# Optimization experiments

Hardware: AMD Instinct MI355X
Metric: run time of the kernel (lower is better)

The kernel has to match this reference:

```python
import jax, jax.numpy as jnp
import numpy as np

N, M, NBR = 20000, 12, 64
AF, ORIG, H, B, K = 256, 92, 256, 200, 50
N_CONV = 3
EPS = 1e-5


def _bn_train(x, gamma, beta):
    mu = x.mean(0)
    var = x.var(0)  # biased, matches torch BN normalization in train mode
    return (x - mu) * jax.lax.rsqrt(var + EPS) * gamma + beta


def _conv_layer(atom_in, nbr_fea, nbr_idx, w1, b1, w2, b2, gamma, beta):
    n, m = nbr_idx.shape
    m1 = m // 2
    atom_nbr = atom_in[nbr_idx]                     # [N, M, AF]
    atom_u = jnp.broadcast_to(atom_in[:, None, :], (n, m1, atom_in.shape[-1]))
    an1, an2 = atom_nbr[:, :m1], atom_nbr[:, m1:]
    nf1, nf2 = nbr_fea[:, :m1], nbr_fea[:, m1:]
    u1 = jnp.concatenate([atom_u, an1, nf1], axis=2)  # [N, M1, 2*AF+NBR]
    u2 = jnp.concatenate([atom_u, an2, nf2], axis=2)
    g1 = jax.nn.relu(jnp.einsum('nmf,fo->nmo', u1, w1) + b1)
    g2 = jax.nn.softplus(jnp.einsum('nmf,fo->nmo', u2, w1) + b1)
    nbr_sumed = g1.sum(1) + g2.sum(1)               # sum over all M neighbors, [N, 2*AF]
    nbr_sumed = nbr_sumed @ w2 + b2                 # [N, AF]
    nbr_sumed = _bn_train(nbr_sumed, gamma, beta)
    return jax.nn.softplus(atom_in + nbr_sumed)


def setup_inputs() -> dict:
    key = jax.random.key(0)
    ks = jax.random.split(key, 16)
    inp = {
        'atom_fea': jax.random.normal(ks[0], (N, ORIG), jnp.float32),
        'nbr_fea': jax.random.normal(ks[1], (N, M, NBR), jnp.float32),
        'nbr_fea_idx': jax.random.randint(ks[2], (N, M), 0, N),
        'M1_index': jax.random.randint(ks[3], (B * K,), 0, N),
        'seg_ids': jnp.repeat(jnp.arange(B), K),
        'm2_fea': jax.random.normal(ks[4], (B, 4), jnp.float32),
        'emb_w': jax.random.normal(ks[5], (ORIG, AF), jnp.float32) * 0.05,
        'emb_b': jnp.zeros((AF,), jnp.float32),
        'w1': jax.random.normal(ks[6], (N_CONV, 2 * AF + NBR, 2 * AF), jnp.float32) * 0.05,
        'b1': jnp.zeros((N_CONV, 2 * AF), jnp.float32),
        'w2': jax.random.normal(ks[7], (N_CONV, 2 * AF, AF), jnp.float32) * 0.05,
        'b2': jnp.zeros((N_CONV, AF), jnp.float32),
        'gamma': jnp.ones((N_CONV, AF), jnp.float32),
        'beta': jnp.zeros((N_CONV, AF), jnp.float32),
        'fc_w': jax.random.normal(ks[8], (AF + 4, H), jnp.float32) * 0.05,
        'fc_b': jnp.zeros((H,), jnp.float32),
        'out_w': jax.random.normal(ks[9], (H, 1), jnp.float32) * 0.05,
        'out_b': jnp.zeros((1,), jnp.float32),
    }
    return inp


def reference(atom_fea, nbr_fea, nbr_fea_idx, M1_index, seg_ids, m2_fea,
              emb_w, emb_b, w1, b1, w2, b2, gamma, beta,
              fc_w, fc_b, out_w, out_b):
    x = jax.nn.softplus(atom_fea @ emb_w + emb_b)           # [N, AF]
    for i in range(N_CONV):
        x = _conv_layer(x, nbr_fea, nbr_fea_idx, w1[i], b1[i], w2[i], b2[i], gamma[i], beta[i])
    m1_fea = x[M1_index]                                    # [B*K, AF]
    sums = jax.ops.segment_sum(m1_fea, seg_ids, num_segments=B)
    counts = jax.ops.segment_sum(jnp.ones((m1_fea.shape[0], 1), m1_fea.dtype), seg_ids, num_segments=B)
    crys = sums / counts                                    # per-crystal mean, [B, AF]
    crys = jnp.concatenate([crys, m2_fea], axis=1)          # [B, AF+4]
    h = jax.nn.softplus(jax.nn.softplus(crys) @ fc_w + fc_b)
    out = h @ out_w + out_b                                 # [B, 1]
    return out
```

## Files before the change

### kernel.cpp

```cpp
#include <hip/hip_runtime.h>
#include <hip/hip_bf16.h>


#define N_ATOM 20000
#define AF     256
#define F2     512
#define ORIG   92
#define ORIG_P 96
#define BB     200
#define KK     50
#define BN_EPS 1e-5f
#define ZS2    268

#define OFF_B1   0
#define OFF_B2   1536
#define OFF_GAM  2304
#define OFF_BET  3072
#define OFF_EMBB 3840
#define OFF_FCB  4096
#define OFF_FCW  4352
#define OFF_OW   70912
#define OFF_OB   71168
#define OFF_M2   71169
#define N_SMALL  71969

#define S_AF   (N_ATOM * ORIG_P)
#define S_EMB  (AF * ORIG_P)
#define S_W12  (3 * 1024 * 256)
#define S_W1F  (3 * 512 * 64)
#define S_W2   (3 * AF * F2)
#define S_SM   N_SMALL
#define S_TOT  (S_AF + S_EMB + S_W12 + S_W1F + S_W2 + S_SM)

using bf16x8 = __attribute__((ext_vector_type(8))) short;
using f32x4  = __attribute__((ext_vector_type(4))) float;

__device__ __forceinline__ float bf2f(__hip_bfloat16 v) { return __bfloat162float(v); }
__device__ __forceinline__ __hip_bfloat16 f2bf(float v) { return __float2bfloat16(v); }
__device__ __forceinline__ unsigned short f2bfbits(float f) {
    unsigned u = __float_as_uint(f);
    u += 0x7fffu + ((u >> 16) & 1u);
    return (unsigned short)(u >> 16);
}
__device__ __forceinline__ float bfbits2f(unsigned short u) {
    return __uint_as_float(((unsigned)u) << 16);
}
__device__ __forceinline__ float softplus_f(float x) {
    return fmaxf(x, 0.f) + __logf(1.f + __expf(-fabsf(x)));
}
__device__ __forceinline__ float ld_any(const void* p, long idx, bool isf32) {
    return isf32 ? ((const float*)p)[idx] : bf2f(((const __hip_bfloat16*)p)[idx]);
}

__global__ void detect_dtype(const unsigned* __restrict__ gamma_raw,
                             unsigned* __restrict__ flag) {
    unsigned u = gamma_raw[0];
    flag[0] = ((u & 0xFFFFu) == 0u) ? 1u : 0u;
}

__global__ __launch_bounds__(256) void prep_nf(const void* __restrict__ nf,
                                               const unsigned* __restrict__ dflag,
                                               unsigned* __restrict__ out) {
    bool isf32 = dflag[0] != 0u;
    int idx = blockIdx.x * 256 + threadIdx.x;
    if (idx >= N_ATOM * 12 * 64 / 4) return;
    if (isf32) {
        float4 v = ((const float4*)nf)[idx];
        out[idx * 2]     = (unsigned)f2bfbits(v.x) | ((unsigned)f2bfbits(v.y) << 16);
        out[idx * 2 + 1] = (unsigned)f2bfbits(v.z) | ((unsigned)f2bfbits(v.w) << 16);
    } else {
        ((uint2*)out)[idx] = ((const uint2*)nf)[idx];
    }
}

__global__ __launch_bounds__(256)
void prep_all(const void* af, const void* emb_w, const void* w1, const void* w2,
              const void* b1, const void* b2, const void* gam, const void* bet,
              const void* embb, const void* fcb, const void* fcw,
              const void* ow, const void* ob, const void* m2,
              const unsigned* __restrict__ dflag,
              __hip_bfloat16* __restrict__ af_pad, __hip_bfloat16* __restrict__ embT,
              __hip_bfloat16* __restrict__ w1T2, __hip_bfloat16* __restrict__ w1Tf,
              __hip_bfloat16* __restrict__ w2T, __hip_bfloat16* __restrict__ smalls) {
    bool isf32 = dflag[0] != 0u;
    int i = blockIdx.x * 256 + threadIdx.x;
    if (i < S_AF) {
        int r = i / ORIG_P, k = i - r * ORIG_P;
        af_pad[i] = (k < ORIG) ? f2bf(ld_any(af, (long)r * ORIG + k, isf32)) : f2bf(0.f);
        return;
    }
    i -= S_AF;
    if (i < S_EMB) {
        int n = i / ORIG_P, k = i - n * ORIG_P;
        embT[i] = (k < ORIG) ? f2bf(ld_any(emb_w, (long)k * AF + n, isf32)) : f2bf(0.f);
        return;
    }
    i -= S_EMB;
    if (i < S_W12) {
        int l = i / (1024 * 256); int rem = i - l * (1024 * 256);
        int c = rem / 256, k = rem - c * 256;
        long src = (c < 512) ? ((long)(l * 576 + k) * F2 + c)
                             : ((long)(l * 576 + 256 + k) * F2 + (c - 512));
        w1T2[i] = f2bf(ld_any(w1, src, isf32));
        return;
    }
    i -= S_W12;
    if (i < S_W1F) {
        int l = i / (512 * 64); int rem = i - l * (512 * 64);
        int c = rem / 64, k = rem - c * 64;
        w1Tf[i] = f2bf(ld_any(w1, (long)(l * 576 + 512 + k) * F2 + c, isf32));
        return;
    }
    i -= S_W1F;
    if (i < S_W2) {
        int l = i / (AF * F2); int rem = i - l * (AF * F2);
        int n = rem / F2, k = rem - n * F2;
        w2T[i] = f2bf(ld_any(w2, (long)(l * F2 + k) * AF + n, isf32));
        return;
    }
    i -= S_W2;
    if (i >= S_SM) return;
    float v;
    if      (i < OFF_B2)   v = ld_any(b1,   i - OFF_B1,  isf32);
    else if (i < OFF_GAM)  v = ld_any(b2,   i - OFF_B2,  isf32);
    else if (i < OFF_BET)  v = ld_any(gam,  i - OFF_GAM, isf32);
    else if (i < OFF_EMBB) v = ld_any(bet,  i - OFF_BET, isf32);
    else if (i < OFF_FCB)  v = ld_any(embb, i - OFF_EMBB,isf32);
    else if (i < OFF_OW)   v = (i < OFF_FCW) ? ld_any(fcb, i - OFF_FCB, isf32)
                                             : ld_any(fcw, i - OFF_FCW, isf32);
    else if (i < OFF_OB)   v = ld_any(ow,   i - OFF_OW,  isf32);
    else if (i < OFF_M2)   v = ld_any(ob,   i - OFF_OB,  isf32);
    else                   v = ld_any(m2,   i - OFF_M2,  isf32);
    smalls[i] = f2bf(v);
}

template <bool OUT_BF16>
__global__ __launch_bounds__(256)
void gemm_kernel(const __hip_bfloat16* __restrict__ A, int lda,
                 const __hip_bfloat16* __restrict__ BT, int ldb,
                 void* __restrict__ Cp, int M, int ldc, int K,
                 const __hip_bfloat16* __restrict__ bias, int act,
                 float* __restrict__ st) {
    __shared__ __align__(16) unsigned short sA[128 * 40];
    __shared__ __align__(16) unsigned short sB[128 * 40];
    __shared__ float sS[128], sS2[128];
    int tid  = threadIdx.x;
    int mt   = blockIdx.x, nt = blockIdx.y;
    int wave = tid >> 6, lane = tid & 63, q = lane >> 4, ln = lane & 15;
    int wr   = wave >> 1, wc = wave & 1;

    if (st && tid < 128) { sS[tid] = 0.f; sS2[tid] = 0.f; }

    f32x4 acc[4][4];
    for (int i = 0; i < 4; i++)
        for (int j = 0; j < 4; j++) acc[i][j] = (f32x4){0.f, 0.f, 0.f, 0.f};

    for (int k0 = 0; k0 < K; k0 += 32) {
        for (int i = tid; i < 512; i += 256) {
            int r = i >> 2, ch = i & 3;
            int row = mt * 128 + r;
            uint4 va = make_uint4(0u, 0u, 0u, 0u);
            if (row < M) va = *(const uint4*)(A + (size_t)row * lda + k0 + ch * 8);
            *(uint4*)(&sA[r * 40 + ch * 8]) = va;
            int n = nt * 128 + r;
            uint4 vb = *(const uint4*)(BT + (size_t)n * ldb + k0 + ch * 8);
            *(uint4*)(&sB[r * 40 + ch * 8]) = vb;
        }
        __syncthreads();
        bf16x8 af[4], bf[4];
        for (int i = 0; i < 4; i++)
            af[i] = *(const bf16x8*)(&sA[(wr * 64 + i * 16 + ln) * 40 + q * 8]);
        for (int j = 0; j < 4; j++)
            bf[j] = *(const bf16x8*)(&sB[(wc * 64 + j * 16 + ln) * 40 + q * 8]);
        for (int i = 0; i < 4; i++)
            for (int j = 0; j < 4; j++)
                acc[i][j] = __builtin_amdgcn_mfma_f32_16x16x32_bf16(af[i], bf[j], acc[i][j], 0, 0, 0);
        __syncthreads();
    }
    for (int j = 0; j < 4; j++) {
        int cl  = wc * 64 + j * 16 + ln;
        int col = nt * 128 + cl;
        float bv = bias ? bf2f(bias[col]) : 0.f;
        float ls = 0.f, ls2 = 0.f;
        for (int i = 0; i < 4; i++) {
            for (int r = 0; r < 4; r++) {
                int row = mt * 128 + wr * 64 + i * 16 + q * 4 + r;
                if (row >= M) continue;
                float v = acc[i][j][r] + bv;
                if (st) { ls += v; ls2 += v * v; }
                if (act == 1) v = softplus_f(v);
                if (OUT_BF16) ((__hip_bfloat16*)Cp)[(size_t)row * ldc + col] = f2bf(v);
                else          ((float*)Cp)[(size_t)row * ldc + col] = v;
            }
        }
        if (st) { atomicAdd(&sS[cl], ls); atomicAdd(&sS2[cl], ls2); }
    }
    if (st) {
        __syncthreads();
        if (tid < 128) {
            int col = nt * 128 + tid;
            atomicAdd(&st[col], sS[tid]);
            atomicAdd(&st[AF + col], sS2[tid]);
        }
    }
}

__global__ __launch_bounds__(256)
void conv_fused(const void* __restrict__ nf,
                const unsigned* __restrict__ dflag,
                int prepped,
                const int* __restrict__ nidx,
                const __hip_bfloat16* __restrict__ xay,
                const __hip_bfloat16* __restrict__ b1l,
                const __hip_bfloat16* __restrict__ w1TfL,
                __hip_bfloat16* __restrict__ ns)
{
    __shared__ __align__(16) unsigned short sNF[48 * 72];
    __shared__ __align__(16) unsigned short sZ[48 * ZS2];
    __shared__ int sIdx[48];

    int tid = threadIdx.x;
    int ab  = blockIdx.x * 4;

    if (prepped || dflag[0] == 0u) {
        const __hip_bfloat16* nfB = (const __hip_bfloat16*)nf;
        for (int i = tid; i < 48 * 8; i += 256) {
            int r = i >> 3, ch = i & 7;
            uint4 v = *(const uint4*)(nfB + (size_t)(ab * 12 + r) * 64 + ch * 8);
            *(uint4*)(&sNF[r * 72 + ch * 8]) = v;
        }
    } else {
        const float* nfF = (const float*)nf;
        for (int i = tid; i < 48 * 8; i += 256) {
            int r = i >> 3, ch = i & 7;
            const float* src = nfF + (size_t)(ab * 12 + r) * 64 + ch * 8;
            float4 v0 = *(const float4*)(src);
            float4 v1 = *(const float4*)(src + 4);
            unsigned short* d = &sNF[r * 72 + ch * 8];
            d[0] = f2bfbits(v0.x); d[1] = f2bfbits(v0.y);
            d[2] = f2bfbits(v0.z); d[3] = f2bfbits(v0.w);
            d[4] = f2bfbits(v1.x); d[5] = f2bfbits(v1.y);
            d[6] = f2bfbits(v1.z); d[7] = f2bfbits(v1.w);
        }
    }
    if (tid < 48) sIdx[tid] = nidx[ab * 12 + tid];
    __syncthreads();

    int wave = tid >> 6, lane = tid & 63, q = lane >> 4, ln = lane & 15;
    int c0 = wave * 32;
    int a = wave, half = lane >> 5, lc = lane & 31;
    int n = ab + a;
    int zc = half * 128 + lc * 4;

    for (int tp = 0; tp < 2; tp++) {
        if (tp) __syncthreads();
        for (int t2 = 0; t2 < 2; t2++) {
            int cb = (tp * 2 + t2) * 128;
            bf16x8 bfr[2][2];
            for (int c2 = 0; c2 < 2; c2++)
                for (int ks = 0; ks < 2; ks++)
                    bfr[c2][ks] = *(const bf16x8*)(w1TfL +
                        (size_t)(cb + c0 + c2 * 16 + ln) * 64 + ks * 32 + q * 8);
            f32x4 acc[3][2];
            for (int rt = 0; rt < 3; rt++)
                for (int c2 = 0; c2 < 2; c2++) acc[rt][c2] = (f32x4){0.f, 0.f, 0.f, 0.f};
            for (int rt = 0; rt < 3; rt++) {
                bf16x8 a0 = *(const bf16x8*)(&sNF[(rt * 16 + ln) * 72 + q * 8]);
                bf16x8 a1 = *(const bf16x8*)(&sNF[(rt * 16 + ln) * 72 + 32 + q * 8]);
                acc[rt][0] = __builtin_amdgcn_mfma_f32_16x16x32_bf16(a0, bfr[0][0], acc[rt][0], 0, 0, 0);
                acc[rt][0] = __builtin_amdgcn_mfma_f32_16x16x32_bf16(a1, bfr[0][1], acc[rt][0], 0, 0, 0);
                acc[rt][1] = __builtin_amdgcn_mfma_f32_16x16x32_bf16(a0, bfr[1][0], acc[rt][1], 0, 0, 0);
                acc[rt][1] = __builtin_amdgcn_mfma_f32_16x16x32_bf16(a1, bfr[1][1], acc[rt][1], 0, 0, 0);
            }
            for (int rt = 0; rt < 3; rt++)
                for (int c2 = 0; c2 < 2; c2++)
                    for (int r = 0; r < 4; r++)
                        sZ[(rt * 16 + q * 4 + r) * ZS2 + t2 * 128 + c0 + c2 * 16 + ln] =
                            f2bfbits(acc[rt][c2][r]);
        }
        __syncthreads();

        int gc = tp * 256 + zc;
        uint2 xau = *(const uint2*)(xay + (size_t)n * 1024 + gc);
        uint2 b1u = *(const uint2*)(b1l + gc);
        float xa0 = bfbits2f((unsigned short)(xau.x & 0xffff)) +
                    bfbits2f((unsigned short)(b1u.x & 0xffff));
        float xa1 = bfbits2f((unsigned short)(xau.x >> 16)) +
                    bfbits2f((unsigned short)(b1u.x >> 16));
        float xa2 = bfbits2f((unsigned short)(xau.y & 0xffff)) +
                    bfbits2f((unsigned short)(b1u.y & 0xffff));
        float xa3 = bfbits2f((unsigned short)(xau.y >> 16)) +
                    bfbits2f((unsigned short)(b1u.y >> 16));
        float r0 = 0.f, r1 = 0.f, r2 = 0.f, r3 = 0.f;
#pragma unroll
        for (int m = 0; m < 12; m++) {
            int gi = sIdx[a * 12 + m];
            uint2 zz = *(const uint2*)(&sZ[(a * 12 + m) * ZS2 + zc]);
            uint2 yy = *(const uint2*)(xay + (size_t)gi * 1024 + 512 + gc);
            float v0 = bfbits2f((unsigned short)(zz.x & 0xffff)) + xa0 +
                       bfbits2f((unsigned short)(yy.x & 0xffff));
            float v1 = bfbits2f((unsigned short)(zz.x >> 16)) + xa1 +
                       bfbits2f((unsigned short)(yy.x >> 16));
            float v2 = bfbits2f((unsigned short)(zz.y & 0xffff)) + xa2 +
                       bfbits2f((unsigned short)(yy.y & 0xffff));
            float v3 = bfbits2f((unsigned short)(zz.y >> 16)) + xa3 +
                       bfbits2f((unsigned short)(yy.y >> 16));
            if (m < 6) {
                v0 = fmaxf(v0, 0.f); v1 = fmaxf(v1, 0.f);
                v2 = fmaxf(v2, 0.f); v3 = fmaxf(v3, 0.f);
            } else {
                v0 = softplus_f(v0); v1 = softplus_f(v1);
                v2 = softplus_f(v2); v3 = softplus_f(v3);
            }
            r0 += v0; r1 += v1; r2 += v2; r3 += v3;
        }
        uint2 o;
        o.x = (unsigned)f2bfbits(r0) | ((unsigned)f2bfbits(r1) << 16);
        o.y = (unsigned)f2bfbits(r2) | ((unsigned)f2bfbits(r3) << 16);
        *(uint2*)(ns + (size_t)n * F2 + gc) = o;
    }
}

__global__ __launch_bounds__(256)
void bn_apply(const __hip_bfloat16* __restrict__ h2, const float* __restrict__ st,
              const __hip_bfloat16* __restrict__ x,
              const __hip_bfloat16* __restrict__ gamma,
              const __hip_bfloat16* __restrict__ beta,
              __hip_bfloat16* __restrict__ xo) {
    int i = (blockIdx.x * 256 + threadIdx.x) * 8;
    int c = i & 255;
    uint4 hv = *(const uint4*)(h2 + i);
    uint4 xv = *(const uint4*)(x + i);
    unsigned hw[4] = {hv.x, hv.y, hv.z, hv.w};
    unsigned xw[4] = {xv.x, xv.y, xv.z, xv.w};
    unsigned ow[4];
    float r[8];
#pragma unroll
    for (int k = 0; k < 8; k++) {
        int cc = c + k;
        float mu  = st[cc] * (1.f / 20000.f);
        float var = fmaxf(st[AF + cc] * (1.f / 20000.f) - mu * mu, 0.f);
        unsigned hh = hw[k >> 1], xx = xw[k >> 1];
        float h  = bfbits2f((unsigned short)((k & 1) ? (hh >> 16) : (hh & 0xffff)));
        float xf = bfbits2f((unsigned short)((k & 1) ? (xx >> 16) : (xx & 0xffff)));
        float t = (h - mu) * rsqrtf(var + BN_EPS) * bf2f(gamma[cc]) + bf2f(beta[cc]);
        r[k] = softplus_f(xf + t);
    }
#pragma unroll
    for (int k = 0; k < 4; k++)
        ow[k] = (unsigned)f2bfbits(r[2 * k]) | ((unsigned)f2bfbits(r[2 * k + 1]) << 16);
    *(uint4*)(xo + i) = make_uint4(ow[0], ow[1], ow[2], ow[3]);
}

__global__ __launch_bounds__(256)
void readout(const __hip_bfloat16* __restrict__ x, const int* __restrict__ m1,
             const __hip_bfloat16* __restrict__ smalls,
             const unsigned* __restrict__ dflag,
             void* __restrict__ outp) {
    __shared__ float sc[AF + 4];
    __shared__ float sred[4];
    bool isf32 = dflag[0] != 0u;
    int b = blockIdx.x, tid = threadIdx.x;
    float s = 0.f;
    for (int j = 0; j < KK; j++) {
        int row = m1[b * KK + j];
        s += bf2f(x[(size_t)row * AF + tid]);
    }
    sc[tid] = softplus_f(s * (1.f / (float)KK));
    if (tid < 4) sc[AF + tid] = softplus_f(bf2f(smalls[OFF_M2 + b * 4 + tid]));
    __syncthreads();
    float acc = bf2f(smalls[OFF_FCB + tid]);
    for (int k = 0; k < AF + 4; k++) acc += sc[k] * bf2f(smalls[OFF_FCW + k * 256 + tid]);
    float h = softplus_f(acc);
    float v = h * bf2f(smalls[OFF_OW + tid]);
    for (int off = 32; off > 0; off >>= 1) v += __shfl_down(v, off);
    if ((tid & 63) == 0) sred[tid >> 6] = v;
    __syncthreads();
    if (tid == 0) {
        float o = sred[0] + sred[1] + sred[2] + sred[3] + bf2f(smalls[OFF_OB]);
        if (isf32) ((float*)outp)[b] = o;
        else       ((__hip_bfloat16*)outp)[b] = f2bf(o);
    }
}

extern "C" void kernel_launch(void* const* d_in, const int* in_sizes, int n_in,
                              void* d_out, int out_size, void* d_ws, size_t ws_size,
                              hipStream_t stream) {
    const void* atom_fea = d_in[0];
    const void* nbr_fea  = d_in[1];
    const int*  nbr_idx  = (const int*)d_in[2];
    const int*  m1_idx   = (const int*)d_in[3];
    const void* m2_fea = d_in[5];
    const void* emb_w  = d_in[6];
    const void* emb_b  = d_in[7];
    const void* w1     = d_in[8];
    const void* b1     = d_in[9];
    const void* w2     = d_in[10];
    const void* b2     = d_in[11];
    const void* gamma  = d_in[12];
    const void* beta   = d_in[13];
    const void* fc_w   = d_in[14];
    const void* fc_b   = d_in[15];
    const void* out_w  = d_in[16];
    const void* out_b  = d_in[17];

    char* ws = (char*)d_ws;
    size_t off = 0;
    auto alloc = [&](size_t bytes) -> char* {
        char* p = ws + off;
        off += (bytes + 255) & ~(size_t)255;
        return p;
    };
    __hip_bfloat16* w1T2   = (__hip_bfloat16*)alloc((size_t)S_W12 * 2);
    __hip_bfloat16* w1Tf   = (__hip_bfloat16*)alloc((size_t)S_W1F * 2);
    __hip_bfloat16* w2T    = (__hip_bfloat16*)alloc((size_t)S_W2 * 2);
    __hip_bfloat16* smalls = (__hip_bfloat16*)alloc((size_t)N_SMALL * 2);
    __hip_bfloat16* xb0    = (__hip_bfloat16*)alloc((size_t)N_ATOM * AF * 2);
    __hip_bfloat16* xb1    = (__hip_bfloat16*)alloc((size_t)N_ATOM * AF * 2);
    char*           regXY  = alloc((size_t)N_ATOM * 1024 * 2);
    char*           regZ   = alloc((size_t)N_ATOM * F2 * 2);
    float*          stats  = (float*)alloc((size_t)3 * 2 * AF * 4);
    unsigned*       dflag  = (unsigned*)alloc(256);
    char*           nfb    = alloc((size_t)N_ATOM * 12 * 64 * 2);
    int use_nfb = (ws_size >= off) ? 1 : 0;

    __hip_bfloat16* xay    = (__hip_bfloat16*)regXY;
    __hip_bfloat16* h2     = (__hip_bfloat16*)regXY;
    __hip_bfloat16* af_pad = (__hip_bfloat16*)(regXY + (size_t)N_ATOM * F2 * 2);
    __hip_bfloat16* embT   = (__hip_bfloat16*)regZ;
    __hip_bfloat16* nsb    = (__hip_bfloat16*)regZ;

    detect_dtype<<<1, 1, 0, stream>>>((const unsigned*)gamma, dflag);
    (void)hipMemsetAsync(stats, 0, (size_t)3 * 2 * AF * 4, stream);

    if (use_nfb)
        prep_nf<<<(N_ATOM * 12 * 64 / 4 + 255) / 256, 256, 0, stream>>>(nbr_fea, dflag,
                                                                        (unsigned*)nfb);
    prep_all<<<(S_TOT + 255) / 256, 256, 0, stream>>>(
        atom_fea, emb_w, w1, w2, b1, b2, gamma, beta, emb_b, fc_b, fc_w,
        out_w, out_b, m2_fea, dflag, af_pad, embT, w1T2, w1Tf, w2T, smalls);

    dim3 g_emb((N_ATOM + 127) / 128, 2);
    gemm_kernel<true><<<g_emb, 256, 0, stream>>>(af_pad, ORIG_P, embT, ORIG_P,
                                                 xb0, N_ATOM, AF, ORIG_P,
                                                 smalls + OFF_EMBB, 1, nullptr);

    const void* nf_conv = use_nfb ? (const void*)nfb : nbr_fea;

    __hip_bfloat16* xc = xb0;
    __hip_bfloat16* xn = xb1;
    for (int l = 0; l < 3; l++) {
        dim3 gxy((N_ATOM + 127) / 128, 8);
        gemm_kernel<true><<<gxy, 256, 0, stream>>>(xc, AF, w1T2 + (size_t)l * 1024 * 256, 256,
                                                   xay, N_ATOM, 1024, AF, nullptr, 0, nullptr);
        conv_fused<<<N_ATOM / 4, 256, 0, stream>>>(nf_conv, dflag, use_nfb, nbr_idx, xay,
                                                   smalls + OFF_B1 + l * F2,
                                                   w1Tf + (size_t)l * 512 * 64, nsb);
        float* stl = stats + l * 2 * AF;
        dim3 gh2((N_ATOM + 127) / 128, 2);
        gemm_kernel<true><<<gh2, 256, 0, stream>>>(nsb, F2, w2T + (size_t)l * AF * F2, F2,
                                                   h2, N_ATOM, AF, F2,
                                                   smalls + OFF_B2 + l * AF, 0, stl);
        bn_apply<<<(N_ATOM * AF / 8) / 256, 256, 0, stream>>>(h2, stl, xc,
                                                              smalls + OFF_GAM + l * AF,
                                                              smalls + OFF_BET + l * AF, xn);
        __hip_bfloat16* t = xc; xc = xn; xn = t;
    }
    readout<<<BB, 256, 0, stream>>>(xc, m1_idx, smalls, dflag, d_out);
}
```

Measured before the change: 622.5 us.

## Pack MFMA outputs as bf16 pairs in LDS and prefetch neighbor gathers

Stores the conv_fused MFMA results into shared memory as packed 32-bit bf16 pairs interleaving the two column tiles, and remaps lanes so each thread reads a uint4 and extracts its half with v_perm. All twelve neighbor-row gathers are issued up front into registers from precomputed byte offsets, and a launch-bounds occupancy hint of 5 is added. A perm-based pack2bf helper replaces the shift-or packing everywhere. Together these aim to cut LDS store count and ds instructions and hide gather latency, at the cost of more registers and a harder-to-verify column mapping.

Measured after the change: 607.6 us. -2.4%, faster.

```diff
diff --git a/kernel.cpp b/kernel.cpp
--- a/kernel.cpp
+++ b/kernel.cpp
@@ -10,7 +10,7 @@
 #define BB     200
 #define KK     50
 #define BN_EPS 1e-5f
-#define ZS2    268
+#define ZPS    132
 
 #define OFF_B1   0
 #define OFF_B2   1536
@@ -45,6 +45,13 @@
 __device__ __forceinline__ float bfbits2f(unsigned short u) {
     return __uint_as_float(((unsigned)u) << 16);
 }
+__device__ __forceinline__ unsigned pack2bf(float lo, float hi) {
+    unsigned ul = __float_as_uint(lo);
+    unsigned uh = __float_as_uint(hi);
+    ul += 0x7fffu + ((ul >> 16) & 1u);
+    uh += 0x7fffu + ((uh >> 16) & 1u);
+    return __builtin_amdgcn_perm(uh, ul, 0x07060302u);
+}
 __device__ __forceinline__ float softplus_f(float x) {
     return fmaxf(x, 0.f) + __logf(1.f + __expf(-fabsf(x)));
 }
@@ -66,8 +73,8 @@
     if (idx >= N_ATOM * 12 * 64 / 4) return;
     if (isf32) {
         float4 v = ((const float4*)nf)[idx];
-        out[idx * 2]     = (unsigned)f2bfbits(v.x) | ((unsigned)f2bfbits(v.y) << 16);
-        out[idx * 2 + 1] = (unsigned)f2bfbits(v.z) | ((unsigned)f2bfbits(v.w) << 16);
+        out[idx * 2]     = pack2bf(v.x, v.y);
+        out[idx * 2 + 1] = pack2bf(v.z, v.w);
     } else {
         ((uint2*)out)[idx] = ((const uint2*)nf)[idx];
     }
@@ -205,7 +212,7 @@
     }
 }
 
-__global__ __launch_bounds__(256)
+__global__ __launch_bounds__(256, 5)
 void conv_fused(const void* __restrict__ nf,
                 const unsigned* __restrict__ dflag,
                 int prepped,
@@ -216,7 +223,7 @@
                 __hip_bfloat16* __restrict__ ns)
 {
     __shared__ __align__(16) unsigned short sNF[48 * 72];
-    __shared__ __align__(16) unsigned short sZ[48 * ZS2];
+    __shared__ __align__(16) unsigned       sZp[48 * ZPS];
     __shared__ int sIdx[48];
 
     int tid = threadIdx.x;
@@ -236,21 +243,31 @@
             const float* src = nfF + (size_t)(ab * 12 + r) * 64 + ch * 8;
             float4 v0 = *(const float4*)(src);
             float4 v1 = *(const float4*)(src + 4);
-            unsigned short* d = &sNF[r * 72 + ch * 8];
-            d[0] = f2bfbits(v0.x); d[1] = f2bfbits(v0.y);
-            d[2] = f2bfbits(v0.z); d[3] = f2bfbits(v0.w);
-            d[4] = f2bfbits(v1.x); d[5] = f2bfbits(v1.y);
-            d[6] = f2bfbits(v1.z); d[7] = f2bfbits(v1.w);
+            unsigned* d = (unsigned*)&sNF[r * 72 + ch * 8];
+            d[0] = pack2bf(v0.x, v0.y);
+            d[1] = pack2bf(v0.z, v0.w);
+            d[2] = pack2bf(v1.x, v1.y);
+            d[3] = pack2bf(v1.z, v1.w);
         }
     }
     if (tid < 48) sIdx[tid] = nidx[ab * 12 + tid];
     __syncthreads();
 
     int wave = tid >> 6, lane = tid & 63, q = lane >> 4, ln = lane & 15;
-    int c0 = wave * 32;
-    int a = wave, half = lane >> 5, lc = lane & 31;
-    int n = ab + a;
-    int zc = half * 128 + lc * 4;
+    int c0  = wave * 32;
+    int c0h = wave * 16;
+    int a = wave, n = ab + a;
+
+    int j5    = lane & 31, c2sel = lane >> 5;
+    int t2r   = (j5 >> 4) & 1, wr2 = (j5 >> 2) & 3, lb = j5 & 3;
+    int ub    = t2r * 64 + wr2 * 16 + lb * 4;
+    int gcp   = t2r * 128 + wr2 * 32 + c2sel * 16 + lb * 4;
+    unsigned sel = c2sel ? 0x03020c0cu : 0x01000c0cu;
+
+    unsigned offm[12];
+#pragma unroll
+    for (int m = 0; m < 12; m++)
+        offm[m] = ((unsigned)sIdx[a * 12 + m] << 11) + 1024u;
 
     for (int tp = 0; tp < 2; tp++) {
         if (tp) __syncthreads();
@@ -272,15 +289,20 @@
                 acc[rt][1] = __builtin_amdgcn_mfma_f32_16x16x32_bf16(a0, bfr[1][0], acc[rt][1], 0, 0, 0);
                 acc[rt][1] = __builtin_amdgcn_mfma_f32_16x16x32_bf16(a1, bfr[1][1], acc[rt][1], 0, 0, 0);
             }
+#pragma unroll
             for (int rt = 0; rt < 3; rt++)
-                for (int c2 = 0; c2 < 2; c2++)
-                    for (int r = 0; r < 4; r++)
-                        sZ[(rt * 16 + q * 4 + r) * ZS2 + t2 * 128 + c0 + c2 * 16 + ln] =
-                            f2bfbits(acc[rt][c2][r]);
+#pragma unroll
+                for (int r = 0; r < 4; r++)
+                    sZp[(rt * 16 + q * 4 + r) * ZPS + t2 * 64 + c0h + ln] =
+                        pack2bf(acc[rt][0][r], acc[rt][1][r]);
         }
         __syncthreads();
 
-        int gc = tp * 256 + zc;
+        int gc = tp * 256 + gcp;
+        uint2 yy[12];
+#pragma unroll
+        for (int m = 0; m < 12; m++)
+            yy[m] = *(const uint2*)((const char*)xay + offm[m] + gc * 2);
         uint2 xau = *(const uint2*)(xay + (size_t)n * 1024 + gc);
         uint2 b1u = *(const uint2*)(b1l + gc);
         float xa0 = bfbits2f((unsigned short)(xau.x & 0xffff)) +
@@ -294,17 +316,15 @@
         float r0 = 0.f, r1 = 0.f, r2 = 0.f, r3 = 0.f;
 #pragma unroll
         for (int m = 0; m < 12; m++) {
-            int gi = sIdx[a * 12 + m];
-            uint2 zz = *(const uint2*)(&sZ[(a * 12 + m) * ZS2 + zc]);
-            uint2 yy = *(const uint2*)(xay + (size_t)gi * 1024 + 512 + gc);
-            float v0 = bfbits2f((unsigned short)(zz.x & 0xffff)) + xa0 +
-                       bfbits2f((unsigned short)(yy.x & 0xffff));
-            float v1 = bfbits2f((unsigned short)(zz.x >> 16)) + xa1 +
-                       bfbits2f((unsigned short)(yy.x >> 16));
-            float v2 = bfbits2f((unsigned short)(zz.y & 0xffff)) + xa2 +
-                       bfbits2f((unsigned short)(yy.y & 0xffff));
-            float v3 = bfbits2f((unsigned short)(zz.y >> 16)) + xa3 +
-                       bfbits2f((unsigned short)(yy.y >> 16));
+            uint4 zz = *(const uint4*)(&sZp[(a * 12 + m) * ZPS + ub]);
+            float v0 = __uint_as_float(__builtin_amdgcn_perm(zz.x, zz.x, sel)) + xa0 +
+                       __uint_as_float(yy[m].x << 16);
+            float v1 = __uint_as_float(__builtin_amdgcn_perm(zz.y, zz.y, sel)) + xa1 +
+                       __uint_as_float(yy[m].x & 0xffff0000u);
+            float v2 = __uint_as_float(__builtin_amdgcn_perm(zz.z, zz.z, sel)) + xa2 +
+                       __uint_as_float(yy[m].y << 16);
+            float v3 = __uint_as_float(__builtin_amdgcn_perm(zz.w, zz.w, sel)) + xa3 +
+                       __uint_as_float(yy[m].y & 0xffff0000u);
             if (m < 6) {
                 v0 = fmaxf(v0, 0.f); v1 = fmaxf(v1, 0.f);
                 v2 = fmaxf(v2, 0.f); v3 = fmaxf(v3, 0.f);
@@ -315,8 +335,8 @@
             r0 += v0; r1 += v1; r2 += v2; r3 += v3;
         }
         uint2 o;
-        o.x = (unsigned)f2bfbits(r0) | ((unsigned)f2bfbits(r1) << 16);
-        o.y = (unsigned)f2bfbits(r2) | ((unsigned)f2bfbits(r3) << 16);
+        o.x = pack2bf(r0, r1);
+        o.y = pack2bf(r2, r3);
         *(uint2*)(ns + (size_t)n * F2 + gc) = o;
     }
 }
@@ -348,7 +368,7 @@
     }
 #pragma unroll
     for (int k = 0; k < 4; k++)
-        ow[k] = (unsigned)f2bfbits(r[2 * k]) | ((unsigned)f2bfbits(r[2 * k + 1]) << 16);
+        ow[k] = pack2bf(r[2 * k], r[2 * k + 1]);
     *(uint4*)(xo + i) = make_uint4(ow[0], ow[1], ow[2], ow[3]);
 }
 
```
